# Kernel optimization log

Hardware: AMD Instinct MI355X
Metric: run time of the kernel (lower is better)

Reference implementation:

```python
import jax, jax.numpy as jnp
import numpy as np

N_NODES = 50000
N_GRAPHS = 128


def gcn_conv(x, W, b, src, dst, n_nodes):
    """PyG-style GCNConv: add self-loops, symmetric normalization, linear transform, scatter-add."""
    # linear transform first (PyG applies lin before propagate)
    h = x @ W  # [N, out]
    loop = jnp.arange(n_nodes, dtype=src.dtype)
    src_f = jnp.concatenate([src, loop])  # [E+N]
    dst_f = jnp.concatenate([dst, loop])
    # degree over destination (incl. self-loops), edge weight = 1
    deg = jax.ops.segment_sum(jnp.ones_like(src_f, dtype=h.dtype), dst_f, num_segments=n_nodes)
    dinv = jnp.where(deg > 0, jax.lax.rsqrt(deg), 0.0)
    norm = dinv[src_f] * dinv[dst_f]  # [E+N]
    msg = h[src_f] * norm[:, None]  # gather + scale
    out = jax.ops.segment_sum(msg, dst_f, num_segments=n_nodes)  # scatter-add
    return out + b


def setup_inputs() -> dict:
    key = jax.random.key(0)
    k = jax.random.split(key, 8)
    in_c, hid_c, out_c = 128, 128, 64
    x = jax.random.normal(k[0], (N_NODES, in_c), dtype=jnp.float32)
    edge_index = jax.random.randint(k[1], (2, 625000), 0, N_NODES, dtype=jnp.int64)
    batch = jnp.sort(jax.random.randint(k[2], (N_NODES,), 0, N_GRAPHS, dtype=jnp.int64))
    # Glorot-style init for GCN weights, zero bias (PyG default)
    W1 = jax.random.normal(k[3], (in_c, hid_c), dtype=jnp.float32) / np.sqrt(in_c)
    b1 = jnp.zeros((hid_c,), dtype=jnp.float32)
    W2 = jax.random.normal(k[4], (hid_c, out_c), dtype=jnp.float32) / np.sqrt(hid_c)
    b2 = jnp.zeros((out_c,), dtype=jnp.float32)
    return {"x": x, "W1": W1, "b1": b1, "W2": W2, "b2": b2,
            "edge_index": edge_index, "batch": batch}


def reference(x, W1, b1, W2, b2, edge_index, batch):
    src, dst = edge_index[0], edge_index[1]
    h = gcn_conv(x, W1, b1, src, dst, N_NODES)
    h = jax.nn.relu(h)
    h = gcn_conv(h, W2, b2, src, dst, N_NODES)  # [N, out_c]
    # global_mean_pool: segment mean over batch vector
    sums = jax.ops.segment_sum(h, batch, num_segments=N_GRAPHS)  # [G, out_c]
    counts = jax.ops.segment_sum(jnp.ones((h.shape[0],), dtype=h.dtype), batch, num_segments=N_GRAPHS)
    return sums / jnp.maximum(counts, 1.0)[:, None]
```

## Files before the change

kernel.cpp:

```cpp
#include <hip/hip_runtime.h>
#include <hip/hip_bf16.h>
#include <hip/hip_fp8.h>
#include <stdint.h>

typedef __hip_bfloat16  bf16;
typedef __hip_bfloat162 bf2;

typedef __attribute__((ext_vector_type(8))) short short8v;
typedef __attribute__((ext_vector_type(4))) float float4v;

#define KSLOT 48
#define CSTRIDE 16

static __device__ __forceinline__ uint32_t pack2(float a, float b) {
  bf2 t = __float22bfloat162_rn(make_float2(a, b));
  return *(uint32_t*)&t;
}
static __device__ __forceinline__ float fp8_to_f(unsigned char b) {
  __hip_fp8_e4m3 t; t.__x = (__hip_fp8_storage_t)b; return (float)t;
}
static __device__ __forceinline__ unsigned char f_to_fp8(float f) {
  __hip_fp8_e4m3 t(f); return (unsigned char)t.__x;
}

union U16x8 { uint32_t u[4]; uint4 q; short8v v; };

#define NB_FILL 306
#define NB_GEMM 782
#define NZB 196


__global__ void k_prep(const float* __restrict__ W1, const float* __restrict__ W2,
                       ushort* __restrict__ Ws1, ushort* __restrict__ Ws2,
                       const int* __restrict__ batch, int* __restrict__ gstart,
                       float* __restrict__ inv_ng, const float* __restrict__ b2,
                       float* __restrict__ out, int* __restrict__ cntS, int n, int G) {
  const int tid = threadIdx.x;
  const int bid = blockIdx.x;
  if (bid == 0) {
    for (int idx = tid; idx < 2048; idx += 256) {
      int t = idx >> 8, c = (idx >> 6) & 3, l = idx & 63;
      int kbase = c * 32 + (l >> 4) * 8, colg = t * 16 + (l & 15);
      U16x8 u;
#pragma unroll
      for (int j = 0; j < 4; ++j)
        u.u[j] = pack2(W1[(size_t)(kbase + 2 * j) * 128 + colg],
                       W1[(size_t)(kbase + 2 * j + 1) * 128 + colg]);
      *(uint4*)&Ws1[(size_t)idx * 8] = u.q;
    }
  } else if (bid == 1) {
    __shared__ int gs[129];
    for (int idx = tid; idx < 1024; idx += 256) {
      int t = idx >> 8, c = (idx >> 6) & 3, l = idx & 63;
      int kbase = c * 32 + (l >> 4) * 8, colg = t * 16 + (l & 15);
      U16x8 u;
#pragma unroll
      for (int j = 0; j < 4; ++j)
        u.u[j] = pack2(W2[(size_t)(kbase + 2 * j) * 64 + colg],
                       W2[(size_t)(kbase + 2 * j + 1) * 64 + colg]);
      *(uint4*)&Ws2[(size_t)idx * 8] = u.q;
    }
    if (tid <= G) {
      int lo = 0, hi = n;
      while (lo < hi) {
        int mid = (lo + hi) >> 1;
        if (batch[mid] < tid) lo = mid + 1; else hi = mid;
      }
      gstart[tid] = lo;
      gs[tid] = lo;
    }
    __syncthreads();
    if (tid < G) inv_ng[tid] = 1.f / (float)max(gs[tid + 1] - gs[tid], 1);
    for (int i = tid; i < G * 64; i += 256) out[i] = b2[i & 63];
  } else {
    int b = bid - 2;
    for (int i = tid; i < 1024; i += 256) {
      int idx4 = b * 1024 + i;
      if (idx4 < 200000) *(uint4*)&cntS[idx4 * 4] = make_uint4(0, 0, 0, 0);
    }
  }
}


__global__ __launch_bounds__(256) void k_fused(
    const float* __restrict__ A, const ushort* __restrict__ Ws1,
    unsigned char* __restrict__ C, int n,
    const int* __restrict__ src, const int* __restrict__ dst,
    int* __restrict__ cntS, ushort* __restrict__ slots, int E) {
  __shared__ ushort Wf[2048 * 8];
  const int bid = blockIdx.x;
  const int tid = threadIdx.x;

  if (bid < NB_FILL) {
    int base = bid * 2048 + tid;
#pragma unroll
    for (int j = 0; j < 8; ++j) {
      int e = base + j * 256;
      if (e < E) {
        int d = dst[e];
        int p = atomicAdd(&cntS[d << 4], 1);
        if (p < KSLOT) slots[(size_t)d * KSLOT + p] = (ushort)src[e];
      }
    }
  } else {
    for (int idx = tid; idx < 2048; idx += 256)
      *(uint4*)&Wf[(size_t)idx * 8] = *(const uint4*)&Ws1[(size_t)idx * 8];
    __syncthreads();
    const int row0 = (bid - NB_FILL) * 64;
    const int w = tid >> 6, lane = tid & 63;
    const int m = lane & 15, q = lane >> 4;
    const int gr = row0 + w * 16 + m;
    float4v acc[8];
#pragma unroll
    for (int t = 0; t < 8; ++t) acc[t] = (float4v){0.f, 0.f, 0.f, 0.f};
    for (int c = 0; c < 4; ++c) {
      U16x8 a;
      if (gr < n) {
        const float* ap = &A[(size_t)gr * 128 + c * 32 + q * 8];
        float4 f0 = *(const float4*)ap;
        float4 f1 = *(const float4*)(ap + 4);
        a.u[0] = pack2(f0.x, f0.y); a.u[1] = pack2(f0.z, f0.w);
        a.u[2] = pack2(f1.x, f1.y); a.u[3] = pack2(f1.z, f1.w);
      } else {
        a.q = make_uint4(0, 0, 0, 0);
      }
#pragma unroll
      for (int t = 0; t < 8; ++t) {
        U16x8 b;
        b.q = *(const uint4*)&Wf[((size_t)(t * 4 + c) * 64 + lane) * 8];
        acc[t] = __builtin_amdgcn_mfma_f32_16x16x32_bf16(a.v, b.v, acc[t], 0, 0, 0);
      }
    }
#pragma unroll
    for (int reg = 0; reg < 4; ++reg) {
      int gor = row0 + w * 16 + q * 4 + reg;
      if (gor < n) {
#pragma unroll
        for (int t = 0; t < 8; ++t)
          C[(size_t)gor * 128 + t * 16 + m] = f_to_fp8(acc[t][reg]);
      }
    }
  }
}

__global__ void k_dinv(const int* __restrict__ cntS, float* __restrict__ dinv, int n) {
  int i = blockIdx.x * blockDim.x + threadIdx.x;
  if (i < n) dinv[i] = rsqrtf((float)(cntS[i << 4] + 1));
}


#define A1STR 136
__global__ __launch_bounds__(256) void k_ag1g2(
    const unsigned char* __restrict__ h, const float* __restrict__ dinv,
    const int* __restrict__ cntS, const ushort* __restrict__ slots,
    const float* __restrict__ b1, const ushort* __restrict__ Ws2,
    unsigned char* __restrict__ H2, int n) {
  __shared__ ushort Wf[1024 * 8];
  __shared__ ushort a1s[16 * A1STR];
  const int tid = threadIdx.x;
  const int wid = tid >> 6, lane = tid & 63;
  const int base = blockIdx.x * 16;

  for (int idx = tid; idx < 1024; idx += 256)
    *(uint4*)&Wf[(size_t)idx * 8] = *(const uint4*)&Ws2[(size_t)idx * 8];

  float2 bb = ((const float2*)b1)[lane];
  for (int s = 0; s < 4; ++s) {
    int nl = wid * 4 + s;
    int v = base + nl;
    if (v < n) {
      float dv = dinv[v];
      ushort sraw = ((const ushort*)(h + (size_t)v * 128))[lane];
      float ax = fp8_to_f((unsigned char)(sraw & 0xff)) * dv;
      float ay = fp8_to_f((unsigned char)(sraw >> 8)) * dv;
      int deg = min(cntS[v << 4], KSLOT);
      const ushort* sl = slots + (size_t)v * KSLOT;
      for (int e = 0; e < deg; e += 8) {
        uint4 u8 = *(const uint4*)&sl[e];
        int id[8] = {(int)(u8.x & 0xffff), (int)(u8.x >> 16), (int)(u8.y & 0xffff), (int)(u8.y >> 16),
                     (int)(u8.z & 0xffff), (int)(u8.z >> 16), (int)(u8.w & 0xffff), (int)(u8.w >> 16)};
        float w[8];
#pragma unroll
        for (int j = 0; j < 8; ++j) {
          bool live = (e + j < deg);
          id[j] = live ? id[j] : v;
          w[j] = live ? dinv[id[j]] : 0.f;
        }
        ushort raw[8];
#pragma unroll
        for (int j = 0; j < 8; ++j)
          raw[j] = ((const ushort*)(h + (size_t)id[j] * 128))[lane];
#pragma unroll
        for (int j = 0; j < 8; ++j) {
          ax += w[j] * fp8_to_f((unsigned char)(raw[j] & 0xff));
          ay += w[j] * fp8_to_f((unsigned char)(raw[j] >> 8));
        }
      }
      float rx = fmaxf(ax * dv + bb.x, 0.f);
      float ry = fmaxf(ay * dv + bb.y, 0.f);
      *(uint32_t*)&a1s[nl * A1STR + lane * 2] = pack2(rx, ry);
    }
  }
  __syncthreads();

  const int m = lane & 15, q = lane >> 4;
  float4v acc = (float4v){0.f, 0.f, 0.f, 0.f};
  for (int c = 0; c < 4; ++c) {
    U16x8 a, b;
    a.q = *(const uint4*)&a1s[m * A1STR + c * 32 + q * 8];
    b.q = *(const uint4*)&Wf[((size_t)(wid * 4 + c) * 64 + lane) * 8];
    acc = __builtin_amdgcn_mfma_f32_16x16x32_bf16(a.v, b.v, acc, 0, 0, 0);
  }
#pragma unroll
  for (int reg = 0; reg < 4; ++reg) {
    int gor = base + q * 4 + reg;
    if (gor < n) H2[(size_t)gor * 64 + wid * 16 + m] = f_to_fp8(acc[reg]);
  }
}


__global__ __launch_bounds__(256) void k_ag2p(
    const unsigned char* __restrict__ h, const float* __restrict__ dinv,
    const int* __restrict__ cntS, const ushort* __restrict__ slots,
    const int* __restrict__ batch, const float* __restrict__ inv_ng,
    float* __restrict__ out, int n) {
  int wid = threadIdx.x >> 6, lane = threadIdx.x & 63;
  int v0 = blockIdx.x * 32 + wid * 8;
  float racc = 0.f;
  int gcur = -1;
  for (int s = 0; s < 8; ++s) {
    int v = v0 + s;
    if (v >= n) break;
    float dv = dinv[v];
    float acc = fp8_to_f(h[(size_t)v * 64 + lane]) * dv;
    int deg = min(cntS[v << 4], KSLOT);
    const ushort* sl = slots + (size_t)v * KSLOT;
    for (int e = 0; e < deg; e += 8) {
      uint4 u8 = *(const uint4*)&sl[e];
      int id[8] = {(int)(u8.x & 0xffff), (int)(u8.x >> 16), (int)(u8.y & 0xffff), (int)(u8.y >> 16),
                   (int)(u8.z & 0xffff), (int)(u8.z >> 16), (int)(u8.w & 0xffff), (int)(u8.w >> 16)};
      float w[8];
#pragma unroll
      for (int j = 0; j < 8; ++j) {
        bool live = (e + j < deg);
        id[j] = live ? id[j] : v;
        w[j] = live ? dinv[id[j]] : 0.f;
      }
      unsigned char raw[8];
#pragma unroll
      for (int j = 0; j < 8; ++j)
        raw[j] = h[(size_t)id[j] * 64 + lane];
#pragma unroll
      for (int j = 0; j < 8; ++j) acc += w[j] * fp8_to_f(raw[j]);
    }
    int g = batch[v];
    if (g != gcur) {
      if (gcur >= 0) atomicAdd(&out[(size_t)gcur * 64 + lane], racc * inv_ng[gcur]);
      gcur = g;
      racc = 0.f;
    }
    racc += acc * dv;
  }
  if (gcur >= 0) atomicAdd(&out[(size_t)gcur * 64 + lane], racc * inv_ng[gcur]);
}


extern "C" void kernel_launch(void* const* d_in, const int* in_sizes, int n_in,
                              void* d_out, int out_size, void* d_ws, size_t ws_size,
                              hipStream_t stream) {
  const float* x   = (const float*)d_in[0];
  const float* W1  = (const float*)d_in[1];
  const float* b1  = (const float*)d_in[2];
  const float* W2  = (const float*)d_in[3];
  const float* b2  = (const float*)d_in[4];
  const int* ei    = (const int*)d_in[5];
  const int* batch = (const int*)d_in[6];

  const int n = in_sizes[0] / 128;
  const int E = in_sizes[5] / 2;
  const int G = 128;

  const int* src = ei;
  const int* dst = ei + E;

  char* ws = (char*)d_ws;
  size_t off = 0;
  auto alloc = [&](size_t bytes) -> void* {
    void* p = ws + off;
    off = (off + bytes + 255) & ~(size_t)255;
    return p;
  };
  unsigned char* h1 = (unsigned char*)alloc((size_t)n * 128);
  unsigned char* H2 = (unsigned char*)alloc((size_t)n * 64);
  ushort* slots = (ushort*)alloc((size_t)n * KSLOT * 2);
  int*    cntS  = (int*)alloc((size_t)n * CSTRIDE * 4);
  float*  dinv  = (float*)alloc((size_t)n * 4);
  int*    gstart= (int*)alloc((size_t)(G + 1) * 4);
  float*  invng = (float*)alloc((size_t)G * 4);
  ushort* Ws1   = (ushort*)alloc(2048 * 16);
  ushort* Ws2   = (ushort*)alloc(1024 * 16);
  float*  out = (float*)d_out;

  k_prep<<<2 + NZB, 256, 0, stream>>>(W1, W2, Ws1, Ws2, batch, gstart, invng, b2,
                                      out, cntS, n, G);
  k_fused<<<NB_FILL + NB_GEMM, 256, 0, stream>>>(x, Ws1, h1, n, src, dst, cntS, slots, E);
  k_dinv<<<(n + 255) / 256, 256, 0, stream>>>(cntS, dinv, n);
  k_ag1g2<<<(n + 15) / 16, 256, 0, stream>>>(h1, dinv, cntS, slots, b1, Ws2, H2, n);
  k_ag2p<<<(n + 31) / 32, 256, 0, stream>>>(H2, dinv, cntS, slots, batch, invng, out, n);
}
```

Before: 178.5 us.

## Gather neighbor rows with 8-byte lanes and split edges across lane groups

Both aggregation kernels change how lanes map to work. Each lane now loads 8 fp8 features per neighbor as one 8-byte load, and different lane groups handle different edges. Partial sums are then combined with cross-lane shuffle reductions. This replaces many narrow 1-2 byte loads per edge with fewer, wider loads and cuts per-lane index and weight handling, at the cost of shuffle reductions, more registers, and idle lanes when a node has few edges.

```diff
diff --git a/kernel.cpp b/kernel.cpp
--- a/kernel.cpp
+++ b/kernel.cpp
@@ -21,6 +21,12 @@
 }
 static __device__ __forceinline__ unsigned char f_to_fp8(float f) {
   __hip_fp8_e4m3 t(f); return (unsigned char)t.__x;
+}
+static __device__ __forceinline__ void unpack8(uint2 raw, float* v) {
+#pragma unroll
+  for (int k = 0; k < 4; ++k) v[k]     = fp8_to_f((unsigned char)((raw.x >> (8 * k)) & 0xff));
+#pragma unroll
+  for (int k = 0; k < 4; ++k) v[4 + k] = fp8_to_f((unsigned char)((raw.y >> (8 * k)) & 0xff));
 }
 
 union U16x8 { uint32_t u[4]; uint4 q; short8v v; };
@@ -160,45 +166,56 @@
   const int tid = threadIdx.x;
   const int wid = tid >> 6, lane = tid & 63;
   const int base = blockIdx.x * 16;
+  const int fg = lane & 15;
+  const int rg = lane >> 4;
 
   for (int idx = tid; idx < 1024; idx += 256)
     *(uint4*)&Wf[(size_t)idx * 8] = *(const uint4*)&Ws2[(size_t)idx * 8];
 
-  float2 bb = ((const float2*)b1)[lane];
   for (int s = 0; s < 4; ++s) {
     int nl = wid * 4 + s;
     int v = base + nl;
     if (v < n) {
       float dv = dinv[v];
-      ushort sraw = ((const ushort*)(h + (size_t)v * 128))[lane];
-      float ax = fp8_to_f((unsigned char)(sraw & 0xff)) * dv;
-      float ay = fp8_to_f((unsigned char)(sraw >> 8)) * dv;
+      float facc[8];
+      {
+        uint2 sraw = *(const uint2*)&h[(size_t)v * 128 + fg * 8];
+        float sv[8]; unpack8(sraw, sv);
+        float sw = (rg == 0) ? dv : 0.f;
+#pragma unroll
+        for (int k = 0; k < 8; ++k) facc[k] = sw * sv[k];
+      }
       int deg = min(cntS[v << 4], KSLOT);
       const ushort* sl = slots + (size_t)v * KSLOT;
-      for (int e = 0; e < deg; e += 8) {
-        uint4 u8 = *(const uint4*)&sl[e];
-        int id[8] = {(int)(u8.x & 0xffff), (int)(u8.x >> 16), (int)(u8.y & 0xffff), (int)(u8.y >> 16),
-                     (int)(u8.z & 0xffff), (int)(u8.z >> 16), (int)(u8.w & 0xffff), (int)(u8.w >> 16)};
-        float w[8];
-#pragma unroll
-        for (int j = 0; j < 8; ++j) {
-          bool live = (e + j < deg);
-          id[j] = live ? id[j] : v;
-          w[j] = live ? dinv[id[j]] : 0.f;
-        }
-        ushort raw[8];
-#pragma unroll
-        for (int j = 0; j < 8; ++j)
-          raw[j] = ((const ushort*)(h + (size_t)id[j] * 128))[lane];
-#pragma unroll
-        for (int j = 0; j < 8; ++j) {
-          ax += w[j] * fp8_to_f((unsigned char)(raw[j] & 0xff));
-          ay += w[j] * fp8_to_f((unsigned char)(raw[j] >> 8));
-        }
-      }
-      float rx = fmaxf(ax * dv + bb.x, 0.f);
-      float ry = fmaxf(ay * dv + bb.y, 0.f);
-      *(uint32_t*)&a1s[nl * A1STR + lane * 2] = pack2(rx, ry);
+      for (int e = 0; e < deg; e += 4) {
+        uint2 s4 = *(const uint2*)&sl[e];
+        uint word = (rg & 2) ? s4.y : s4.x;
+        int myid = (rg & 1) ? (int)(word >> 16) : (int)(word & 0xffff);
+        bool live = (e + rg < deg);
+        myid = live ? myid : v;
+        float w = live ? dinv[myid] : 0.f;
+        uint2 raw = *(const uint2*)&h[(size_t)myid * 128 + fg * 8];
+        float gv[8]; unpack8(raw, gv);
+#pragma unroll
+        for (int k = 0; k < 8; ++k) facc[k] += w * gv[k];
+      }
+#pragma unroll
+      for (int k = 0; k < 8; ++k) facc[k] += __shfl_xor(facc[k], 16);
+#pragma unroll
+      for (int k = 0; k < 8; ++k) facc[k] += __shfl_xor(facc[k], 32);
+      if (rg == 0) {
+        float4 bA = *(const float4*)&b1[fg * 8];
+        float4 bB = *(const float4*)&b1[fg * 8 + 4];
+        float r[8];
+#pragma unroll
+        for (int k = 0; k < 4; ++k) r[k]     = fmaxf(facc[k] * dv + (&bA.x)[k], 0.f);
+#pragma unroll
+        for (int k = 0; k < 4; ++k) r[4 + k] = fmaxf(facc[4 + k] * dv + (&bB.x)[k], 0.f);
+        uint4 o;
+        o.x = pack2(r[0], r[1]); o.y = pack2(r[2], r[3]);
+        o.z = pack2(r[4], r[5]); o.w = pack2(r[6], r[7]);
+        *(uint4*)&a1s[nl * A1STR + fg * 8] = o;
+      }
     }
   }
   __syncthreads();
@@ -225,43 +242,67 @@
     const int* __restrict__ batch, const float* __restrict__ inv_ng,
     float* __restrict__ out, int n) {
   int wid = threadIdx.x >> 6, lane = threadIdx.x & 63;
+  const int fg = lane & 7;
+  const int rg = lane >> 3;
   int v0 = blockIdx.x * 32 + wid * 8;
-  float racc = 0.f;
+  float racc[8];
+#pragma unroll
+  for (int k = 0; k < 8; ++k) racc[k] = 0.f;
   int gcur = -1;
   for (int s = 0; s < 8; ++s) {
     int v = v0 + s;
     if (v >= n) break;
     float dv = dinv[v];
-    float acc = fp8_to_f(h[(size_t)v * 64 + lane]) * dv;
+    float facc[8];
+    {
+      uint2 sraw = *(const uint2*)&h[(size_t)v * 64 + fg * 8];
+      float sv[8]; unpack8(sraw, sv);
+      float sw = (rg == 0) ? dv : 0.f;
+#pragma unroll
+      for (int k = 0; k < 8; ++k) facc[k] = sw * sv[k];
+    }
     int deg = min(cntS[v << 4], KSLOT);
     const ushort* sl = slots + (size_t)v * KSLOT;
     for (int e = 0; e < deg; e += 8) {
       uint4 u8 = *(const uint4*)&sl[e];
-      int id[8] = {(int)(u8.x & 0xffff), (int)(u8.x >> 16), (int)(u8.y & 0xffff), (int)(u8.y >> 16),
-                   (int)(u8.z & 0xffff), (int)(u8.z >> 16), (int)(u8.w & 0xffff), (int)(u8.w >> 16)};
-      float w[8];
-#pragma unroll
-      for (int j = 0; j < 8; ++j) {
-        bool live = (e + j < deg);
-        id[j] = live ? id[j] : v;
-        w[j] = live ? dinv[id[j]] : 0.f;
-      }
-      unsigned char raw[8];
-#pragma unroll
-      for (int j = 0; j < 8; ++j)
-        raw[j] = h[(size_t)id[j] * 64 + lane];
-#pragma unroll
-      for (int j = 0; j < 8; ++j) acc += w[j] * fp8_to_f(raw[j]);
-    }
+      uint2 half = (rg & 4) ? make_uint2(u8.z, u8.w) : make_uint2(u8.x, u8.y);
+      uint word = (rg & 2) ? half.y : half.x;
+      int myid = (rg & 1) ? (int)(word >> 16) : (int)(word & 0xffff);
+      bool live = (e + rg < deg);
+      myid = live ? myid : v;
+      float w = live ? dinv[myid] : 0.f;
+      uint2 raw = *(const uint2*)&h[(size_t)myid * 64 + fg * 8];
+      float gv[8]; unpack8(raw, gv);
+#pragma unroll
+      for (int k = 0; k < 8; ++k) facc[k] += w * gv[k];
+    }
+#pragma unroll
+    for (int k = 0; k < 8; ++k) facc[k] += __shfl_xor(facc[k], 8);
+#pragma unroll
+    for (int k = 0; k < 8; ++k) facc[k] += __shfl_xor(facc[k], 16);
+#pragma unroll
+    for (int k = 0; k < 8; ++k) facc[k] += __shfl_xor(facc[k], 32);
     int g = batch[v];
     if (g != gcur) {
-      if (gcur >= 0) atomicAdd(&out[(size_t)gcur * 64 + lane], racc * inv_ng[gcur]);
+      if (gcur >= 0 && rg == 0) {
+        float sc = inv_ng[gcur];
+#pragma unroll
+        for (int k = 0; k < 8; ++k)
+          atomicAdd(&out[(size_t)gcur * 64 + fg * 8 + k], racc[k] * sc);
+      }
+#pragma unroll
+      for (int k = 0; k < 8; ++k) racc[k] = 0.f;
       gcur = g;
-      racc = 0.f;
-    }
-    racc += acc * dv;
-  }
-  if (gcur >= 0) atomicAdd(&out[(size_t)gcur * 64 + lane], racc * inv_ng[gcur]);
+    }
+#pragma unroll
+    for (int k = 0; k < 8; ++k) racc[k] += facc[k] * dv;
+  }
+  if (gcur >= 0 && rg == 0) {
+    float sc = inv_ng[gcur];
+#pragma unroll
+    for (int k = 0; k < 8; ++k)
+      atomicAdd(&out[(size_t)gcur * 64 + fg * 8 + k], racc[k] * sc);
+  }
 }
 
 
```

Result: slower. 199.5 us (+11.8%).

## Pre-scale node features by dinv to drop per-edge dinv gathers

Applied to the files above, without the earlier changes.

The source-side normalization dinv[src] is folded into the node features: a new kernel rescales h1 by dinv in place, and the layer-1 output is multiplied by dinv before it is written as H2. The aggregation kernels then use unit weights instead of gathering dinv per neighbor, which removes a random 4-byte load per edge in both layers. In exchange it adds a full read-modify-write pass over h1, and applies an extra fp8 requantization after scaling, which may change numerical error.

```diff
diff --git a/kernel.cpp b/kernel.cpp
--- a/kernel.cpp
+++ b/kernel.cpp
@@ -143,9 +143,41 @@
   }
 }
 
-__global__ void k_dinv(const int* __restrict__ cntS, float* __restrict__ dinv, int n) {
-  int i = blockIdx.x * blockDim.x + threadIdx.x;
-  if (i < n) dinv[i] = rsqrtf((float)(cntS[i << 4] + 1));
+
+__global__ __launch_bounds__(256) void k_dinvs(const int* __restrict__ cntS,
+                                               float* __restrict__ dinv,
+                                               unsigned char* __restrict__ h1, int n) {
+  __shared__ float sd[64];
+  const int base = blockIdx.x * 64;
+  const int tid = threadIdx.x;
+  if (tid < 64) {
+    int i = base + tid;
+    float d = 0.f;
+    if (i < n) { d = rsqrtf((float)(cntS[i << 4] + 1)); dinv[i] = d; }
+    sd[tid] = d;
+  }
+  __syncthreads();
+  for (int u = tid; u < 512; u += 256) {
+    int r = u >> 3, c = u & 7;
+    int i = base + r;
+    if (i < n) {
+      uint4 raw = *(uint4*)&h1[(size_t)i * 128 + c * 16];
+      float s = sd[r];
+      uint in[4] = {raw.x, raw.y, raw.z, raw.w};
+      uint outw[4];
+#pragma unroll
+      for (int w = 0; w < 4; ++w) {
+        uint o = 0;
+#pragma unroll
+        for (int b = 0; b < 4; ++b) {
+          float f = fp8_to_f((unsigned char)((in[w] >> (8 * b)) & 0xff)) * s;
+          o |= ((uint)f_to_fp8(f)) << (8 * b);
+        }
+        outw[w] = o;
+      }
+      *(uint4*)&h1[(size_t)i * 128 + c * 16] = make_uint4(outw[0], outw[1], outw[2], outw[3]);
+    }
+  }
 }
 
 
@@ -171,8 +203,8 @@
     if (v < n) {
       float dv = dinv[v];
       ushort sraw = ((const ushort*)(h + (size_t)v * 128))[lane];
-      float ax = fp8_to_f((unsigned char)(sraw & 0xff)) * dv;
-      float ay = fp8_to_f((unsigned char)(sraw >> 8)) * dv;
+      float ax = fp8_to_f((unsigned char)(sraw & 0xff));
+      float ay = fp8_to_f((unsigned char)(sraw >> 8));
       int deg = min(cntS[v << 4], KSLOT);
       const ushort* sl = slots + (size_t)v * KSLOT;
       for (int e = 0; e < deg; e += 8) {
@@ -184,7 +216,7 @@
         for (int j = 0; j < 8; ++j) {
           bool live = (e + j < deg);
           id[j] = live ? id[j] : v;
-          w[j] = live ? dinv[id[j]] : 0.f;
+          w[j] = live ? 1.f : 0.f;
         }
         ushort raw[8];
 #pragma unroll
@@ -214,7 +246,10 @@
 #pragma unroll
   for (int reg = 0; reg < 4; ++reg) {
     int gor = base + q * 4 + reg;
-    if (gor < n) H2[(size_t)gor * 64 + wid * 16 + m] = f_to_fp8(acc[reg]);
+    if (gor < n) {
+      float dsc = dinv[gor];
+      H2[(size_t)gor * 64 + wid * 16 + m] = f_to_fp8(acc[reg] * dsc);
+    }
   }
 }
 
@@ -232,7 +267,7 @@
     int v = v0 + s;
     if (v >= n) break;
     float dv = dinv[v];
-    float acc = fp8_to_f(h[(size_t)v * 64 + lane]) * dv;
+    float acc = fp8_to_f(h[(size_t)v * 64 + lane]);
     int deg = min(cntS[v << 4], KSLOT);
     const ushort* sl = slots + (size_t)v * KSLOT;
     for (int e = 0; e < deg; e += 8) {
@@ -244,7 +279,7 @@
       for (int j = 0; j < 8; ++j) {
         bool live = (e + j < deg);
         id[j] = live ? id[j] : v;
-        w[j] = live ? dinv[id[j]] : 0.f;
+        w[j] = live ? 1.f : 0.f;
       }
       unsigned char raw[8];
 #pragma unroll
@@ -304,7 +339,7 @@
   k_prep<<<2 + NZB, 256, 0, stream>>>(W1, W2, Ws1, Ws2, batch, gstart, invng, b2,
                                       out, cntS, n, G);
   k_fused<<<NB_FILL + NB_GEMM, 256, 0, stream>>>(x, Ws1, h1, n, src, dst, cntS, slots, E);
-  k_dinv<<<(n + 255) / 256, 256, 0, stream>>>(cntS, dinv, n);
+  k_dinvs<<<(n + 63) / 64, 256, 0, stream>>>(cntS, dinv, h1, n);
   k_ag1g2<<<(n + 15) / 16, 256, 0, stream>>>(h1, dinv, cntS, slots, b1, Ws2, H2, n);
   k_ag2p<<<(n + 31) / 32, 256, 0, stream>>>(H2, dinv, cntS, slots, batch, invng, out, n);
 }
```

After: 177.6 us. Within noise of the previous version (-0.5%).
